# Kernel tuning notes

Measured on AMD Instinct MI355X. Metric: run time of the kernel, lower is better.

The kernel has to match this reference:

```python
import jax, jax.numpy as jnp
import numpy as np

N = 4096
F_IN = 3000
F_OUT = 64
NEG_INF = jnp.float32(-9e15)


def _xavier(key, shape):
    fan_in, fan_out = shape[0], shape[-1]
    limit = (6.0 / (fan_in + fan_out)) ** 0.5
    return jax.random.uniform(key, shape, jnp.float32, -limit, limit)


def setup_inputs() -> dict:
    key = jax.random.key(0)
    ks = jax.random.split(key, 20)
    feat = jax.random.normal(ks[0], (N, F_IN), jnp.float32)
    feat_a = jax.random.normal(ks[1], (N, F_IN), jnp.float32)
    eye = jnp.eye(N, dtype=jnp.float32)
    adj = jnp.maximum((jax.random.uniform(ks[2], (N, N)) < 0.008).astype(jnp.float32), eye)
    graph_neigh = jnp.maximum((jax.random.uniform(ks[3], (N, N)) < 0.008).astype(jnp.float32), eye)
    return {
        "feat": feat,
        "feat_a": feat_a,
        "adj": adj,
        "graph_neigh": graph_neigh,
        "weight1": _xavier(ks[4], (F_IN, F_OUT)),
        "weight2": _xavier(ks[5], (F_OUT, F_IN)),
        "att_W": _xavier(ks[6], (F_OUT, F_OUT)),
        "a_src": _xavier(ks[7], (F_OUT, 1)),
        "a_dst": _xavier(ks[8], (F_OUT, 1)),
        "mlp_W1": _xavier(ks[9], (F_OUT, 256)),
        "mlp_b1": jnp.zeros((256,), jnp.float32),
        "mlp_W2": _xavier(ks[10], (256, 128)),
        "mlp_b2": jnp.zeros((128,), jnp.float32),
        "mlp_W3": _xavier(ks[11], (128, F_OUT)),
        "mlp_b3": jnp.zeros((F_OUT,), jnp.float32),
        "dmlp_W1": _xavier(ks[12], (F_OUT, 128)),
        "dmlp_b1": jnp.zeros((128,), jnp.float32),
        "dmlp_W2": _xavier(ks[13], (128, F_OUT)),
        "dmlp_b2": jnp.zeros((F_OUT,), jnp.float32),
        "bil_W": _xavier(ks[14], (F_OUT, F_OUT)),
        "bil_b": jnp.zeros((1,), jnp.float32),
    }


def reference(feat, feat_a, adj, graph_neigh,
              weight1, weight2, att_W, a_src, a_dst,
              mlp_W1, mlp_b1, mlp_W2, mlp_b2, mlp_W3, mlp_b3,
              dmlp_W1, dmlp_b1, dmlp_W2, dmlp_b2, bil_W, bil_b):
    relu = jax.nn.relu

    def attention(h):
        Wh = h @ att_W                      # [N, F_OUT]
        e = Wh @ a_src + (Wh @ a_dst).T     # [N, N]
        e = jnp.where(e > 0, e, 0.2 * e)    # LeakyReLU(0.2)
        e = jnp.where(adj > 0, e, NEG_INF)  # mask non-edges
        return jax.nn.softmax(e, axis=1) @ Wh

    def mlp(x):
        x = relu(x @ mlp_W1 + mlp_b1)
        x = relu(x @ mlp_W2 + mlp_b2)
        return x @ mlp_W3 + mlp_b3

    def dmlp(x):  # discriminator MLP: n_h -> 128 -> n_h
        return relu(x @ dmlp_W1 + dmlp_b1) @ dmlp_W2 + dmlp_b2

    def readout(emb):  # AvgReadout + L2 normalize
        g = (graph_neigh @ emb) / jnp.sum(graph_neigh, axis=1, keepdims=True)
        return g / jnp.maximum(jnp.linalg.norm(g, axis=1, keepdims=True), 1e-12)

    def bilinear(x, y):  # nn.Bilinear(n_h, n_h, 1)
        return (jnp.einsum('ni,ij,nj->n', x, bil_W, y) + bil_b)[:, None]

    def disc(c, h_pl, h_mi):
        c, h_pl, h_mi = dmlp(c), dmlp(h_pl), dmlp(h_mi)
        return jnp.concatenate([bilinear(h_pl, c), bilinear(h_mi, c)], axis=1)

    z = mlp(attention(feat @ weight1))
    hiden_emb = z
    h = adj @ (z @ weight2)                 # spmm(adj, z @ weight2)
    emb = relu(z)
    z_a = mlp(attention(feat_a @ weight1))
    emb_a = relu(z_a)
    g = jax.nn.sigmoid(readout(emb))
    g_a = jax.nn.sigmoid(readout(emb_a))
    ret = disc(g, emb, emb_a)
    ret_a = disc(g_a, emb_a, emb)
    return (hiden_emb, h, ret, ret_a)
```

## Files before the change

### kernel.cpp

```cpp
#include <hip/hip_runtime.h>

#define NN   4096
#define FIN  3000
#define MAXN 128

typedef unsigned short u16;
typedef __bf16 bf16x8 __attribute__((ext_vector_type(8)));
typedef float f32x16 __attribute__((ext_vector_type(16)));

__device__ __forceinline__ float bf2f(u16 u) { union { unsigned int i; float f; } v; v.i = ((unsigned int)u) << 16; return v.f; }
__device__ __forceinline__ u16 f2bf(float f) {
    union { float f; unsigned int i; } v; v.f = f;
    return (u16)((v.i + 0x7FFFu + ((v.i >> 16) & 1u)) >> 16);
}
__device__ __forceinline__ bf16x8 bzero8() {
    union { unsigned long long q[2]; bf16x8 v; } u; u.q[0] = 0ull; u.q[1] = 0ull; return u.v;
}
__device__ __forceinline__ f32x16 fzero16() {
    f32x16 v;
    #pragma unroll
    for (int i = 0; i < 16; i++) v[i] = 0.f;
    return v;
}
__device__ __forceinline__ void gload_lds16(const float* src, void* ldsbase) {
    __builtin_amdgcn_global_load_lds(
        (const __attribute__((address_space(1))) void*)src,
        (__attribute__((address_space(3))) void*)ldsbase, 16, 0, 0);
}

__global__ __launch_bounds__(1024) void k_detect(const u16* __restrict__ feat, int* __restrict__ flag)
{
    __shared__ int tot;
    if (threadIdx.x == 0) tot = 0;
    __syncthreads();
    int ins = 0;
    for (int i = threadIdx.x; i < 16384; i += 1024) {
        u16 u = feat[i];
        int e = (u >> 7) & 0xFF;
        if (u != 0 && (e < 90 || e > 160)) ins++;
    }
    atomicAdd(&tot, ins);
    __syncthreads();
    if (threadIdx.x == 0) *flag = (tot > 1024) ? 1 : 0;
}

__global__ __launch_bounds__(256) void k_convw(const int* __restrict__ flag,
    const void* s0, const void* s1, const void* s2, const void* s3,
    const void* s4, const void* s5, const void* s6, const void* s7,
    const void* s8, const void* s9, const void* s10, const void* s11,
    const void* s12, const void* s13, const void* s14, const void* s15,
    float* __restrict__ dst)
{
    const void* srcs[16] = {s0,s1,s2,s3,s4,s5,s6,s7,s8,s9,s10,s11,s12,s13,s14,s15};
    const int offs[16] = {0,192000,196096,196160,196224,212608,212864,245632,245760,253952,254016,262208,262336,270528,270592,274688};
    const int ns[16]   = {192000,4096,64,64,16384,256,32768,128,8192,64,8192,128,8192,64,4096,1};
    int seg = blockIdx.y;
    int i = blockIdx.x * 256 + threadIdx.x;
    if (i >= ns[seg]) return;
    float v = (*flag) ? ((const float*)srcs[seg])[i] : bf2f(((const u16*)srcs[seg])[i]);
    dst[offs[seg] + i] = v;
}

__global__ __launch_bounds__(256) void k_convw2t(const int* __restrict__ flag,
    const void* __restrict__ src, u16* __restrict__ WH, u16* __restrict__ WL)
{
    int i = blockIdx.x * 256 + threadIdx.x;
    if (i >= 3008 * 64) return;
    int n = i >> 6, k = i & 63;
    float v = 0.f;
    if (n < FIN)
        v = (*flag) ? ((const float*)src)[(size_t)k * FIN + n]
                    : bf2f(((const u16*)src)[(size_t)k * FIN + n]);
    u16 h = f2bf(v);
    float r = v - bf2f(h);
    WH[i] = h;
    WL[i] = f2bf(r);
}

__global__ __launch_bounds__(256) void k_convw1t(const int* __restrict__ flag,
    const void* __restrict__ w1src, u16* __restrict__ BtH, u16* __restrict__ BtL)
{
    int i = blockIdx.x * 256 + threadIdx.x;
    if (i >= 64 * 3008) return;
    int c = i / 3008, k = i - c * 3008;
    float v = 0.f;
    if (k < 3000)
        v = (*flag) ? ((const float*)w1src)[(size_t)k * 64 + c]
                    : bf2f(((const u16*)w1src)[(size_t)k * 64 + c]);
    u16 h = f2bf(v);
    float r = v - bf2f(h);
    BtH[(size_t)c * 3008 + k] = h;
    BtL[(size_t)c * 3008 + k] = f2bf(r);
}

__global__ __launch_bounds__(256) void k_build_csr(const int* __restrict__ flag,
    const void* __restrict__ Av, const void* __restrict__ Gv,
    int* __restrict__ aCnt, int* __restrict__ aIdx,
    int* __restrict__ gCnt, int* __restrict__ gIdx)
{
    bool isf = (*flag != 0);
    const void* M = blockIdx.y ? Gv : Av;
    int* cnt = blockIdx.y ? gCnt : aCnt;
    int* idx = blockIdx.y ? gIdx : aIdx;
    int row = blockIdx.x, t = threadIdx.x;
    int c0 = t * 16;
    unsigned int mask = 0; int my = 0;
    if (isf) {
        const float4* r = (const float4*)((const float*)M + (size_t)row * NN + c0);
        union { float4 q[4]; float f[16]; } u;
        u.q[0] = r[0]; u.q[1] = r[1]; u.q[2] = r[2]; u.q[3] = r[3];
        #pragma unroll
        for (int j = 0; j < 16; j++) if (u.f[j] != 0.f) { mask |= 1u << j; my++; }
    } else {
        const uint4* r = (const uint4*)((const u16*)M + (size_t)row * NN + c0);
        union { uint4 q[2]; u16 h[16]; } u;
        u.q[0] = r[0]; u.q[1] = r[1];
        #pragma unroll
        for (int j = 0; j < 16; j++) if (u.h[j] != 0) { mask |= 1u << j; my++; }
    }
    __shared__ int sc[256];
    sc[t] = my;
    __syncthreads();
    for (int d = 1; d < 256; d <<= 1) {
        int v = (t >= d) ? sc[t - d] : 0;
        __syncthreads();
        sc[t] += v;
        __syncthreads();
    }
    int pos = sc[t] - my;
    for (int j = 0; j < 16; j++) {
        if (mask & (1u << j)) {
            if (pos < MAXN) idx[(size_t)row * MAXN + pos] = c0 + j;
            pos++;
        }
    }
    if (t == 0) { int total = sc[255]; cnt[row] = (total < MAXN) ? total : MAXN; }
}

__global__ __launch_bounds__(512) void k_featgemm_mfma(const int* __restrict__ flag,
    const void* __restrict__ F0v, const void* __restrict__ F1v,
    const u16* __restrict__ BtH, float* __restrict__ X0, float* __restrict__ X1)
{
    if (*flag) return;
    const u16* F = (const u16*)(blockIdx.y ? F1v : F0v);
    float* X = blockIdx.y ? X1 : X0;
    int r0 = blockIdx.x * 32;
    int tid = threadIdx.x;
    int w  = tid >> 6;
    int l  = tid & 63;
    int lr = l & 31;
    int kg = l >> 5;
    const u16* arow = F   + (size_t)(r0 + lr) * FIN + kg * 8;
    const u16* b0p  = BtH + (size_t)lr * 3008 + kg * 8;
    const u16* b1p  = BtH + (size_t)(lr + 32) * 3008 + kg * 8;
    f32x16 acc0 = fzero16(), acc1 = fzero16();
    #pragma unroll 4
    for (int s = w; s < 188; s += 8) {
        int kk = s * 16;
        bf16x8 a;
        if (kk + kg * 8 < FIN) a = *(const bf16x8*)(arow + kk);
        else                   a = bzero8();
        bf16x8 b0 = *(const bf16x8*)(b0p + kk);
        bf16x8 b1 = *(const bf16x8*)(b1p + kk);
        acc0 = __builtin_amdgcn_mfma_f32_32x32x16_bf16(a, b0, acc0, 0, 0, 0);
        acc1 = __builtin_amdgcn_mfma_f32_32x32x16_bf16(a, b1, acc1, 0, 0, 0);
    }
    __shared__ float red[8][2048];
    float* rp = red[w];
    #pragma unroll
    for (int reg = 0; reg < 16; reg++) {
        int row = (reg & 3) + 8 * (reg >> 2) + 4 * kg;
        rp[row * 64 + lr] = acc0[reg];
    }
    #pragma unroll
    for (int reg = 0; reg < 16; reg++) {
        int row = (reg & 3) + 8 * (reg >> 2) + 4 * kg;
        rp[row * 64 + 32 + lr] = acc1[reg];
    }
    __syncthreads();
    for (int i = tid; i < 2048; i += 512) {
        float s0 = 0.f;
        #pragma unroll
        for (int j = 0; j < 8; j++) s0 += red[j][i];
        X[(size_t)r0 * 64 + i] = s0;
    }
}

__global__ __launch_bounds__(256) void k_featgemm_mfma_f32(const int* __restrict__ flag,
    const void* __restrict__ F0v, const void* __restrict__ F1v,
    const u16* __restrict__ BtH, const u16* __restrict__ BtL,
    float* __restrict__ X0, float* __restrict__ X1)
{
    if (!*flag) return;
    const float* F = (const float*)(blockIdx.y ? F1v : F0v);
    float* X = blockIdx.y ? X1 : X0;
    int tid = threadIdx.x;
    int w  = tid >> 6;
    int l  = tid & 63;
    int lr = l & 31;
    int kg = l >> 5;
    int wr = w >> 1, wc = w & 1;
    int r0 = blockIdx.x * 64;
    int chunk = blockIdx.z;
    int sbeg = chunk * 12;
    int nsteps = ((chunk == 3) ? 47 : sbeg + 12) - sbeg;

    __shared__ char lds[2][16384];

    const float* Fb = F + (size_t)r0 * FIN;
    int arow = 32 * wr + lr;
    int acol = 32 * wc + lr;
    const u16* bh = BtH + (size_t)acol * 3008;
    const u16* bl = BtL + (size_t)acol * 3008;

    int slin = (w * 16) * 256 + l * 16;
    f32x16 acc = fzero16();

    {
        int kbase = sbeg * 64;
        #pragma unroll
        for (int j = 0; j < 4; j++) {
            int lin = slin + j * 1024;
            int row = lin >> 8;
            int off = (lin & 255) ^ ((row & 15) << 4);
            gload_lds16(Fb + (size_t)row * FIN + kbase + (off >> 2),
                        &lds[0][(w * 16 + j * 4) * 256]);
        }
    }
    __syncthreads();

    int cur = 0;
    for (int s = 0; s < nsteps; ++s) {
        if (s + 1 < nsteps) {
            int kbase = (sbeg + s + 1) * 64;
            #pragma unroll
            for (int j = 0; j < 4; j++) {
                int lin = slin + j * 1024;
                int row = lin >> 8;
                int off = (lin & 255) ^ ((row & 15) << 4);
                gload_lds16(Fb + (size_t)row * FIN + kbase + (off >> 2),
                            &lds[cur ^ 1][(w * 16 + j * 4) * 256]);
            }
        }
        const char* lb = lds[cur];
        int kk0 = (sbeg + s) * 64;
        #pragma unroll
        for (int s16 = 0; s16 < 4; s16++) {
            int offu = s16 * 64 + kg * 32;
            int o0 = offu        ^ ((arow & 15) << 4);
            int o1 = (offu + 16) ^ ((arow & 15) << 4);
            float4 a0 = *(const float4*)(lb + arow * 256 + o0);
            float4 a1 = *(const float4*)(lb + arow * 256 + o1);
            float av[8] = {a0.x, a0.y, a0.z, a0.w, a1.x, a1.y, a1.z, a1.w};
            bf16x8 ah, al;
            #pragma unroll
            for (int jj = 0; jj < 8; jj++) {
                __bf16 hv = (__bf16)av[jj];
                ah[jj] = hv;
                al[jj] = (__bf16)(av[jj] - (float)hv);
            }
            int kk = kk0 + s16 * 16 + kg * 8;
            bf16x8 H = *(const bf16x8*)(bh + kk);
            bf16x8 L = *(const bf16x8*)(bl + kk);
            acc = __builtin_amdgcn_mfma_f32_32x32x16_bf16(ah, H, acc, 0, 0, 0);
            acc = __builtin_amdgcn_mfma_f32_32x32x16_bf16(al, H, acc, 0, 0, 0);
            acc = __builtin_amdgcn_mfma_f32_32x32x16_bf16(ah, L, acc, 0, 0, 0);
        }
        __syncthreads();
        cur ^= 1;
    }

    #pragma unroll
    for (int reg = 0; reg < 16; reg++) {
        int row = (reg & 3) + 8 * (reg >> 2) + 4 * kg;
        atomicAdd(&X[(size_t)(r0 + 32 * wr + row) * 64 + acol], acc[reg]);
    }
}

__global__ __launch_bounds__(64) void k_whsd(
    const float* __restrict__ X1, const float* __restrict__ X2,
    const float* __restrict__ AW, const float* __restrict__ asrc, const float* __restrict__ adst,
    float* __restrict__ Wh1, float* __restrict__ Wh2,
    float* __restrict__ s1, float* __restrict__ s2,
    float* __restrict__ d1, float* __restrict__ d2)
{
    const float* X = blockIdx.y ? X2 : X1;
    float* Wh = blockIdx.y ? Wh2 : Wh1;
    float* sv = blockIdx.y ? s2 : s1;
    float* dv = blockIdx.y ? d2 : d1;
    int row = blockIdx.x, c = threadIdx.x;
    __shared__ float x[64];
    x[c] = X[(size_t)row * 64 + c];
    __syncthreads();
    float acc = 0.f;
    #pragma unroll 16
    for (int k = 0; k < 64; k++) acc += x[k] * AW[k * 64 + c];
    Wh[(size_t)row * 64 + c] = acc;
    float vs = acc * asrc[c];
    float vd = acc * adst[c];
    #pragma unroll
    for (int off = 32; off > 0; off >>= 1) { vs += __shfl_down(vs, off); vd += __shfl_down(vd, off); }
    if (c == 0) { sv[row] = vs; dv[row] = vd; }
}

__global__ __launch_bounds__(128) void k_attn(
    const int* __restrict__ cnt, const int* __restrict__ idx,
    const float* __restrict__ s1, const float* __restrict__ s2,
    const float* __restrict__ d1, const float* __restrict__ d2,
    const float* __restrict__ Wh1, const float* __restrict__ Wh2,
    float* __restrict__ A1, float* __restrict__ A2)
{
    const float* sp = blockIdx.y ? s2 : s1;
    const float* dp = blockIdx.y ? d2 : d1;
    const float* Wh = blockIdx.y ? Wh2 : Wh1;
    float* A = blockIdx.y ? A2 : A1;
    int row = blockIdx.x, tid = threadIdx.x;
    int n = cnt[row];
    __shared__ int js[MAXN];
    __shared__ float ps[MAXN];
    __shared__ float red2[2];
    __shared__ float ared[2][64];
    for (int k = tid; k < n; k += 128) js[k] = idx[(size_t)row * MAXN + k];
    __syncthreads();
    float si = sp[row];
    float m = -3.0e38f;
    for (int k = tid; k < n; k += 128) {
        float e = si + dp[js[k]];
        e = e > 0.f ? e : 0.2f * e;
        ps[k] = e;
        m = fmaxf(m, e);
    }
    #pragma unroll
    for (int off = 32; off > 0; off >>= 1) m = fmaxf(m, __shfl_down(m, off));
    if ((tid & 63) == 0) red2[tid >> 6] = m;
    __syncthreads();
    m = fmaxf(red2[0], red2[1]);
    __syncthreads();
    float zz = 0.f;
    for (int k = tid; k < n; k += 128) {
        float p = __expf(ps[k] - m);
        ps[k] = p;
        zz += p;
    }
    #pragma unroll
    for (int off = 32; off > 0; off >>= 1) zz += __shfl_down(zz, off);
    if ((tid & 63) == 0) red2[tid >> 6] = zz;
    __syncthreads();
    float Z = red2[0] + red2[1];
    Z = fmaxf(Z, 1e-20f);
    int f = tid & 63, half = tid >> 6;
    float acc = 0.f;
    for (int k = half; k < n; k += 2) acc += ps[k] * Wh[(size_t)js[k] * 64 + f];
    ared[half][f] = acc;
    __syncthreads();
    if (tid < 64) A[(size_t)row * 64 + f] = (ared[0][f] + ared[1][f]) / Z;
}

__global__ __launch_bounds__(256) void k_mlp(const int* __restrict__ flag,
    const float* __restrict__ A1, const float* __restrict__ A2,
    const float* __restrict__ W1, const float* __restrict__ b1,
    const float* __restrict__ W2, const float* __restrict__ b2,
    const float* __restrict__ W3, const float* __restrict__ b3,
    float* __restrict__ Z1, float* __restrict__ Z2, void* __restrict__ hidenv)
{
    const float* A = blockIdx.y ? A2 : A1;
    float* Z = blockIdx.y ? Z2 : Z1;
    int row0 = blockIdx.x * 4, tid = threadIdx.x;
    __shared__ float x[4][64], h1[4][256], h2[4][128];
    {
        int r = tid >> 6, c = tid & 63;
        x[r][c] = A[(size_t)(row0 + r) * 64 + c];
    }
    __syncthreads();
    {
        float a0 = b1[tid], a1v = a0, a2v = a0, a3v = a0;
        #pragma unroll 8
        for (int k = 0; k < 64; k++) {
            float w = W1[k * 256 + tid];
            a0 += x[0][k] * w; a1v += x[1][k] * w; a2v += x[2][k] * w; a3v += x[3][k] * w;
        }
        h1[0][tid] = fmaxf(a0, 0.f);  h1[1][tid] = fmaxf(a1v, 0.f);
        h1[2][tid] = fmaxf(a2v, 0.f); h1[3][tid] = fmaxf(a3v, 0.f);
    }
    __syncthreads();
    if (tid < 128) {
        float a0 = b2[tid], a1v = a0, a2v = a0, a3v = a0;
        #pragma unroll 8
        for (int k = 0; k < 256; k++) {
            float w = W2[k * 128 + tid];
            a0 += h1[0][k] * w; a1v += h1[1][k] * w; a2v += h1[2][k] * w; a3v += h1[3][k] * w;
        }
        h2[0][tid] = fmaxf(a0, 0.f);  h2[1][tid] = fmaxf(a1v, 0.f);
        h2[2][tid] = fmaxf(a2v, 0.f); h2[3][tid] = fmaxf(a3v, 0.f);
    }
    __syncthreads();
    if (tid < 64) {
        float a[4];
        a[0] = a[1] = a[2] = a[3] = b3[tid];
        #pragma unroll 8
        for (int k = 0; k < 128; k++) {
            float w = W3[k * 64 + tid];
            a[0] += h2[0][k] * w; a[1] += h2[1][k] * w; a[2] += h2[2][k] * w; a[3] += h2[3][k] * w;
        }
        bool isf = (*flag != 0);
        #pragma unroll
        for (int r = 0; r < 4; r++) {
            size_t ei = (size_t)(row0 + r) * 64 + tid;
            Z[ei] = a[r];
            if (blockIdx.y == 0) {
                if (isf) ((float*)hidenv)[ei] = a[r];
                else     ((u16*)hidenv)[ei] = f2bf(a[r]);
            }
        }
    }
}

__global__ __launch_bounds__(64) void k_spmm(
    const int* __restrict__ cnt, const int* __restrict__ idx,
    const float* __restrict__ Z, float* __restrict__ T)
{
    int row = blockIdx.x, f = threadIdx.x;
    int n = cnt[row];
    const int* ir = idx + (size_t)row * MAXN;
    float acc = 0.f;
    for (int k = 0; k < n; k++) acc += Z[(size_t)ir[k] * 64 + f];
    T[(size_t)row * 64 + f] = acc;
}

__global__ __launch_bounds__(256) void k_hgemm_mfma(const int* __restrict__ flag,
    const float* __restrict__ T, const u16* __restrict__ WH, const u16* __restrict__ WL,
    void* __restrict__ outv)
{
    bool isf = (*flag != 0);
    int tid = threadIdx.x;
    int w = tid >> 6, l = tid & 63, lr = l & 31, kg = l >> 5;
    int ct = blockIdx.y * 4 + w;
    if (ct >= 94) return;
    int r0 = blockIdx.x * 32, c0 = ct * 32;
    const float* tp = T + (size_t)(r0 + lr) * 64 + kg * 8;
    bf16x8 ah[4], al[4];
    #pragma unroll
    for (int s = 0; s < 4; s++) {
        float4 p0 = *(const float4*)(tp + s * 16);
        float4 p1 = *(const float4*)(tp + s * 16 + 4);
        float av[8] = {p0.x, p0.y, p0.z, p0.w, p1.x, p1.y, p1.z, p1.w};
        #pragma unroll
        for (int j = 0; j < 8; j++) {
            __bf16 hv = (__bf16)av[j];
            ah[s][j] = hv;
            al[s][j] = (__bf16)(av[j] - (float)hv);
        }
    }
    const u16* bh = WH + (size_t)(c0 + lr) * 64 + kg * 8;
    const u16* bl = WL + (size_t)(c0 + lr) * 64 + kg * 8;
    f32x16 acc = fzero16();
    #pragma unroll
    for (int s = 0; s < 4; s++) {
        bf16x8 vh = *(const bf16x8*)(bh + s * 16);
        bf16x8 vl = *(const bf16x8*)(bl + s * 16);
        acc = __builtin_amdgcn_mfma_f32_32x32x16_bf16(ah[s], vh, acc, 0, 0, 0);
        acc = __builtin_amdgcn_mfma_f32_32x32x16_bf16(al[s], vh, acc, 0, 0, 0);
        acc = __builtin_amdgcn_mfma_f32_32x32x16_bf16(ah[s], vl, acc, 0, 0, 0);
    }
    int col = c0 + lr;
    bool cok = col < FIN;
    #pragma unroll
    for (int reg = 0; reg < 16; reg++) {
        int row = (reg & 3) + 8 * (reg >> 2) + 4 * kg;
        size_t ei = 262144 + (size_t)(r0 + row) * FIN + col;
        if (cok) {
            if (isf) ((float*)outv)[ei] = acc[reg];
            else     ((u16*)outv)[ei] = f2bf(acc[reg]);
        }
    }
}

__global__ __launch_bounds__(64) void k_readout(
    const int* __restrict__ cnt, const int* __restrict__ idx,
    const float* __restrict__ Z1, const float* __restrict__ Z2,
    float* __restrict__ G1, float* __restrict__ G2)
{
    const float* Z = blockIdx.y ? Z2 : Z1;
    float* G = blockIdx.y ? G2 : G1;
    int row = blockIdx.x, f = threadIdx.x;
    int n = cnt[row];
    const int* ir = idx + (size_t)row * MAXN;
    float acc = 0.f;
    for (int k = 0; k < n; k++) acc += fmaxf(Z[(size_t)ir[k] * 64 + f], 0.f);
    acc /= (float)(n > 0 ? n : 1);
    float sq = acc * acc;
    #pragma unroll
    for (int off = 32; off > 0; off >>= 1) sq += __shfl_down(sq, off);
    sq = __shfl(sq, 0);
    float nrm = fmaxf(sqrtf(sq), 1e-12f);
    float v = acc / nrm;
    G[(size_t)row * 64 + f] = 1.f / (1.f + __expf(-v));
}

__global__ __launch_bounds__(128) void k_dmlp(
    const float* __restrict__ z, const float* __restrict__ za,
    const float* __restrict__ g, const float* __restrict__ ga,
    const float* __restrict__ W1, const float* __restrict__ b1,
    const float* __restrict__ W2, const float* __restrict__ b2,
    float* __restrict__ De, float* __restrict__ Dea,
    float* __restrict__ Dg, float* __restrict__ Dga)
{
    int w = blockIdx.y;
    const float* X = (w == 0) ? z : (w == 1) ? za : (w == 2) ? g : ga;
    float* O = (w == 0) ? De : (w == 1) ? Dea : (w == 2) ? Dg : Dga;
    int doRelu = (w < 2);
    int row0 = blockIdx.x * 4, tid = threadIdx.x;
    __shared__ float x[4][64], h1[4][128];
    for (int i = tid; i < 256; i += 128) {
        int r = i >> 6, c = i & 63;
        float v = X[(size_t)(row0 + r) * 64 + c];
        x[r][c] = doRelu ? fmaxf(v, 0.f) : v;
    }
    __syncthreads();
    {
        float a0 = b1[tid], a1v = a0, a2v = a0, a3v = a0;
        #pragma unroll 8
        for (int k = 0; k < 64; k++) {
            float w_ = W1[k * 128 + tid];
            a0 += x[0][k] * w_; a1v += x[1][k] * w_; a2v += x[2][k] * w_; a3v += x[3][k] * w_;
        }
        h1[0][tid] = fmaxf(a0, 0.f);  h1[1][tid] = fmaxf(a1v, 0.f);
        h1[2][tid] = fmaxf(a2v, 0.f); h1[3][tid] = fmaxf(a3v, 0.f);
    }
    __syncthreads();
    if (tid < 64) {
        float a[4];
        a[0] = a[1] = a[2] = a[3] = b2[tid];
        #pragma unroll 8
        for (int k = 0; k < 128; k++) {
            float w_ = W2[k * 64 + tid];
            a[0] += h1[0][k] * w_; a[1] += h1[1][k] * w_; a[2] += h1[2][k] * w_; a[3] += h1[3][k] * w_;
        }
        #pragma unroll
        for (int r = 0; r < 4; r++) O[(size_t)(row0 + r) * 64 + tid] = a[r];
    }
}

__global__ __launch_bounds__(64) void k_bilin(const int* __restrict__ flag,
    const float* __restrict__ De, const float* __restrict__ Dea,
    const float* __restrict__ Dg, const float* __restrict__ Dga,
    const float* __restrict__ BW, const float* __restrict__ bb, void* __restrict__ outv)
{
    int w = blockIdx.y;
    const float* X = (w == 0 || w == 3) ? De : Dea;
    const float* Y = (w <= 1) ? Dg : Dga;
    size_t bse = (w <= 1) ? (size_t)12550144 : (size_t)12558336;
    int col = (w == 0 || w == 2) ? 0 : 1;
    int row = blockIdx.x, k = threadIdx.x;
    __shared__ float x[64], y[64];
    x[k] = X[(size_t)row * 64 + k];
    y[k] = Y[(size_t)row * 64 + k];
    __syncthreads();
    float wv = 0.f;
    #pragma unroll 8
    for (int j = 0; j < 64; j++) wv += BW[k * 64 + j] * y[j];
    float v = x[k] * wv;
    #pragma unroll
    for (int off = 32; off > 0; off >>= 1) v += __shfl_down(v, off);
    if (k == 0) {
        float r = v + bb[0];
        size_t ei = bse + (size_t)row * 2 + col;
        if (*flag) ((float*)outv)[ei] = r;
        else       ((u16*)outv)[ei] = f2bf(r);
    }
}

extern "C" void kernel_launch(void* const* d_in, const int* in_sizes, int n_in,
                              void* d_out, int out_size, void* d_ws, size_t ws_size,
                              hipStream_t stream) {
    const void* feat   = d_in[0];
    const void* feat_a = d_in[1];
    const void* adj    = d_in[2];
    const void* gn     = d_in[3];
    const void* w1     = d_in[4];
    const void* w2     = d_in[5];
    const void* attW   = d_in[6];
    const void* a_src  = d_in[7];
    const void* a_dst  = d_in[8];
    const void* mW1    = d_in[9];
    const void* mb1    = d_in[10];
    const void* mW2    = d_in[11];
    const void* mb2    = d_in[12];
    const void* mW3    = d_in[13];
    const void* mb3    = d_in[14];
    const void* dW1    = d_in[15];
    const void* db1    = d_in[16];
    const void* dW2    = d_in[17];
    const void* db2    = d_in[18];
    const void* bW     = d_in[19];
    const void* bb     = d_in[20];
    (void)in_sizes; (void)n_in; (void)out_size;

    char* wsb = (char*)d_ws;
    int*   flag = (int*)wsb;
    float* T    = (float*)(wsb + 256);
    u16*   W2tH = (u16*)(wsb + 256 + 1048576);
    u16*   W2tL = W2tH + 3008 * 64;
    (void)ws_size;

    char* sc = (char*)d_out + 1048576;
    size_t soff = 0;
    auto salloc = [&](size_t nbytes) -> void* {
        void* p = (void*)(sc + soff);
        soff += (nbytes + 255) & ~(size_t)255;
        return p;
    };
    const size_t NV = (size_t)NN * 64;
    float* wA   = (float*)salloc((size_t)274689 * 4);
    int*   aCnt = (int*)salloc(NN * 4);
    int*   gCnt = (int*)salloc(NN * 4);
    int*   aIdx = (int*)salloc((size_t)NN * MAXN * 4);
    int*   gIdx = (int*)salloc((size_t)NN * MAXN * 4);
    float* X1  = (float*)salloc(NV * 4);
    float* X2  = (float*)salloc(NV * 4);
    float* Wh1 = (float*)salloc(NV * 4);
    float* Wh2 = (float*)salloc(NV * 4);
    float* A1  = (float*)salloc(NV * 4);
    float* A2  = (float*)salloc(NV * 4);
    float* z   = (float*)salloc(NV * 4);
    float* za  = (float*)salloc(NV * 4);
    float* g   = (float*)salloc(NV * 4);
    float* ga  = (float*)salloc(NV * 4);
    float* De  = (float*)salloc(NV * 4);
    float* Dea = (float*)salloc(NV * 4);
    float* Dg  = (float*)salloc(NV * 4);
    float* Dga = (float*)salloc(NV * 4);
    float* s1  = (float*)salloc(NN * 4);
    float* s2  = (float*)salloc(NN * 4);
    float* d1  = (float*)salloc(NN * 4);
    float* d2  = (float*)salloc(NN * 4);

    float* w1f   = wA + 0;
    float* attWf = wA + 192000;
    float* asrcf = wA + 196096;
    float* adstf = wA + 196160;
    float* mW1f  = wA + 196224;
    float* mb1f  = wA + 212608;
    float* mW2f  = wA + 212864;
    float* mb2f  = wA + 245632;
    float* mW3f  = wA + 245760;
    float* mb3f  = wA + 253952;
    float* dW1f  = wA + 254016;
    float* db1f  = wA + 262208;
    float* dW2f  = wA + 262336;
    float* db2f  = wA + 270528;
    float* bWf   = wA + 270592;
    float* bbf   = wA + 274688;

    u16* BtH = (u16*)De;
    u16* BtL = (u16*)Dea;

    k_detect<<<1, 1024, 0, stream>>>((const u16*)feat, flag);
    k_convw<<<dim3(750, 16), 256, 0, stream>>>(flag,
        w1, attW, a_src, a_dst, mW1, mb1, mW2, mb2, mW3, mb3,
        dW1, db1, dW2, db2, bW, bb, wA);
    k_convw2t<<<752, 256, 0, stream>>>(flag, w2, W2tH, W2tL);
    k_convw1t<<<752, 256, 0, stream>>>(flag, w1, BtH, BtL);
    k_build_csr<<<dim3(NN, 2), 256, 0, stream>>>(flag, adj, gn, aCnt, aIdx, gCnt, gIdx);
    hipMemsetAsync(X1, 0, 2 * NV * 4, stream);
    k_featgemm_mfma<<<dim3(NN / 32, 2), 512, 0, stream>>>(flag, feat, feat_a, BtH, X1, X2);
    k_featgemm_mfma_f32<<<dim3(NN / 64, 2, 4), 256, 0, stream>>>(flag, feat, feat_a, BtH, BtL, X1, X2);
    k_whsd<<<dim3(NN, 2), 64, 0, stream>>>(X1, X2, attWf, asrcf, adstf, Wh1, Wh2, s1, s2, d1, d2);
    k_attn<<<dim3(NN, 2), 128, 0, stream>>>(aCnt, aIdx, s1, s2, d1, d2, Wh1, Wh2, A1, A2);
    k_mlp<<<dim3(NN / 4, 2), 256, 0, stream>>>(flag, A1, A2, mW1f, mb1f, mW2f, mb2f, mW3f, mb3f, z, za, d_out);
    k_readout<<<dim3(NN, 2), 64, 0, stream>>>(gCnt, gIdx, z, za, g, ga);
    k_dmlp<<<dim3(NN / 4, 4), 128, 0, stream>>>(z, za, g, ga, dW1f, db1f, dW2f, db2f, De, Dea, Dg, Dga);
    k_bilin<<<dim3(NN, 4), 64, 0, stream>>>(flag, De, Dea, Dg, Dga, bWf, bbf, d_out);
    k_spmm<<<NN, 64, 0, stream>>>(aCnt, aIdx, z, T);
    k_hgemm_mfma<<<dim3(NN / 32, 24), 256, 0, stream>>>(flag, T, W2tH, W2tL, d_out);
}
```

Baseline: 461.6 us.

## Triple-buffer f32 feature GEMM, batch whsd rows, split bilinear into precompute and dot

```diff
diff --git a/kernel.cpp b/kernel.cpp
--- a/kernel.cpp
+++ b/kernel.cpp
@@ -203,46 +203,39 @@
     int r0 = blockIdx.x * 64;
     int chunk = blockIdx.z;
     int sbeg = chunk * 12;
-    int nsteps = ((chunk == 3) ? 47 : sbeg + 12) - sbeg;
-
-    __shared__ char lds[2][16384];
+    int nsteps = (chunk == 3) ? 11 : 12;
+
+    __shared__ char lds[3][16384];
 
     const float* Fb = F + (size_t)r0 * FIN;
     int arow = 32 * wr + lr;
     int acol = 32 * wc + lr;
     const u16* bh = BtH + (size_t)acol * 3008;
     const u16* bl = BtL + (size_t)acol * 3008;
-
     int slin = (w * 16) * 256 + l * 16;
     f32x16 acc = fzero16();
 
-    {
-        int kbase = sbeg * 64;
+    auto STAGE = [&](int s, int buf) {
+        int kbase = (sbeg + s) * 64;
         #pragma unroll
         for (int j = 0; j < 4; j++) {
             int lin = slin + j * 1024;
             int row = lin >> 8;
             int off = (lin & 255) ^ ((row & 15) << 4);
             gload_lds16(Fb + (size_t)row * FIN + kbase + (off >> 2),
-                        &lds[0][(w * 16 + j * 4) * 256]);
-        }
-    }
-    __syncthreads();
-
-    int cur = 0;
+                        &lds[buf][(w * 16 + j * 4) * 256]);
+        }
+    };
+
+    STAGE(0, 0);
+    STAGE(1, 1);
+
     for (int s = 0; s < nsteps; ++s) {
-        if (s + 1 < nsteps) {
-            int kbase = (sbeg + s + 1) * 64;
-            #pragma unroll
-            for (int j = 0; j < 4; j++) {
-                int lin = slin + j * 1024;
-                int row = lin >> 8;
-                int off = (lin & 255) ^ ((row & 15) << 4);
-                gload_lds16(Fb + (size_t)row * FIN + kbase + (off >> 2),
-                            &lds[cur ^ 1][(w * 16 + j * 4) * 256]);
-            }
-        }
-        const char* lb = lds[cur];
+        if (s < nsteps - 1) asm volatile("s_waitcnt vmcnt(4)" ::: "memory");
+        else                asm volatile("s_waitcnt vmcnt(0)" ::: "memory");
+        __builtin_amdgcn_s_barrier();
+        if (s + 2 < nsteps) STAGE(s + 2, (s + 2) % 3);
+        const char* lb = lds[s % 3];
         int kk0 = (sbeg + s) * 64;
         #pragma unroll
         for (int s16 = 0; s16 < 4; s16++) {
@@ -266,8 +259,6 @@
             acc = __builtin_amdgcn_mfma_f32_32x32x16_bf16(al, H, acc, 0, 0, 0);
             acc = __builtin_amdgcn_mfma_f32_32x32x16_bf16(ah, L, acc, 0, 0, 0);
         }
-        __syncthreads();
-        cur ^= 1;
     }
 
     #pragma unroll
@@ -277,7 +268,7 @@
     }
 }
 
-__global__ __launch_bounds__(64) void k_whsd(
+__global__ __launch_bounds__(256) void k_whsd(
     const float* __restrict__ X1, const float* __restrict__ X2,
     const float* __restrict__ AW, const float* __restrict__ asrc, const float* __restrict__ adst,
     float* __restrict__ Wh1, float* __restrict__ Wh2,
@@ -288,13 +279,17 @@
     float* Wh = blockIdx.y ? Wh2 : Wh1;
     float* sv = blockIdx.y ? s2 : s1;
     float* dv = blockIdx.y ? d2 : d1;
-    int row = blockIdx.x, c = threadIdx.x;
-    __shared__ float x[64];
-    x[c] = X[(size_t)row * 64 + c];
+    __shared__ float aw[64][65];
+    __shared__ float x[4][65];
+    int tid = threadIdx.x;
+    for (int i = tid; i < 4096; i += 256) aw[i >> 6][i & 63] = AW[i];
+    int g = tid >> 6, c = tid & 63;
+    int row = blockIdx.x * 4 + g;
+    x[g][c] = X[(size_t)row * 64 + c];
     __syncthreads();
     float acc = 0.f;
     #pragma unroll 16
-    for (int k = 0; k < 64; k++) acc += x[k] * AW[k * 64 + c];
+    for (int k = 0; k < 64; k++) acc += x[g][k] * aw[k][c];
     Wh[(size_t)row * 64 + c] = acc;
     float vs = acc * asrc[c];
     float vd = acc * adst[c];
@@ -541,25 +536,43 @@
     }
 }
 
-__global__ __launch_bounds__(64) void k_bilin(const int* __restrict__ flag,
+__global__ __launch_bounds__(256) void k_bilin_pre(
+    const float* __restrict__ Dg, const float* __restrict__ Dga,
+    const float* __restrict__ BW, float* __restrict__ V1, float* __restrict__ V2)
+{
+    const float* Y = blockIdx.y ? Dga : Dg;
+    float* V = blockIdx.y ? V2 : V1;
+    __shared__ float bw[64][65];
+    __shared__ float y[4][65];
+    int tid = threadIdx.x;
+    for (int i = tid; i < 4096; i += 256) bw[i >> 6][i & 63] = BW[i];
+    int g = tid >> 6, k = tid & 63;
+    int rbase = blockIdx.x * 64;
+    for (int it = 0; it < 16; it++) {
+        __syncthreads();
+        int r = rbase + it * 4 + g;
+        y[g][k] = Y[(size_t)r * 64 + k];
+        __syncthreads();
+        float acc = 0.f;
+        #pragma unroll 16
+        for (int j = 0; j < 64; j++) acc += y[g][j] * bw[k][j];
+        V[(size_t)r * 64 + k] = acc;
+    }
+}
+
+__global__ __launch_bounds__(256) void k_bilin_dot(const int* __restrict__ flag,
     const float* __restrict__ De, const float* __restrict__ Dea,
-    const float* __restrict__ Dg, const float* __restrict__ Dga,
-    const float* __restrict__ BW, const float* __restrict__ bb, void* __restrict__ outv)
+    const float* __restrict__ V1, const float* __restrict__ V2,
+    const float* __restrict__ bb, void* __restrict__ outv)
 {
     int w = blockIdx.y;
     const float* X = (w == 0 || w == 3) ? De : Dea;
-    const float* Y = (w <= 1) ? Dg : Dga;
+    const float* V = (w <= 1) ? V1 : V2;
     size_t bse = (w <= 1) ? (size_t)12550144 : (size_t)12558336;
     int col = (w == 0 || w == 2) ? 0 : 1;
-    int row = blockIdx.x, k = threadIdx.x;
-    __shared__ float x[64], y[64];
-    x[k] = X[(size_t)row * 64 + k];
-    y[k] = Y[(size_t)row * 64 + k];
-    __syncthreads();
-    float wv = 0.f;
-    #pragma unroll 8
-    for (int j = 0; j < 64; j++) wv += BW[k * 64 + j] * y[j];
-    float v = x[k] * wv;
+    int g = threadIdx.x >> 6, k = threadIdx.x & 63;
+    int row = blockIdx.x * 4 + g;
+    float v = X[(size_t)row * 64 + k] * V[(size_t)row * 64 + k];
     #pragma unroll
     for (int off = 32; off > 0; off >>= 1) v += __shfl_down(v, off);
     if (k == 0) {
@@ -665,12 +678,13 @@
     hipMemsetAsync(X1, 0, 2 * NV * 4, stream);
     k_featgemm_mfma<<<dim3(NN / 32, 2), 512, 0, stream>>>(flag, feat, feat_a, BtH, X1, X2);
     k_featgemm_mfma_f32<<<dim3(NN / 64, 2, 4), 256, 0, stream>>>(flag, feat, feat_a, BtH, BtL, X1, X2);
-    k_whsd<<<dim3(NN, 2), 64, 0, stream>>>(X1, X2, attWf, asrcf, adstf, Wh1, Wh2, s1, s2, d1, d2);
+    k_whsd<<<dim3(NN / 4, 2), 256, 0, stream>>>(X1, X2, attWf, asrcf, adstf, Wh1, Wh2, s1, s2, d1, d2);
     k_attn<<<dim3(NN, 2), 128, 0, stream>>>(aCnt, aIdx, s1, s2, d1, d2, Wh1, Wh2, A1, A2);
     k_mlp<<<dim3(NN / 4, 2), 256, 0, stream>>>(flag, A1, A2, mW1f, mb1f, mW2f, mb2f, mW3f, mb3f, z, za, d_out);
     k_readout<<<dim3(NN, 2), 64, 0, stream>>>(gCnt, gIdx, z, za, g, ga);
     k_dmlp<<<dim3(NN / 4, 4), 128, 0, stream>>>(z, za, g, ga, dW1f, db1f, dW2f, db2f, De, Dea, Dg, Dga);
-    k_bilin<<<dim3(NN, 4), 64, 0, stream>>>(flag, De, Dea, Dg, Dga, bWf, bbf, d_out);
+    k_bilin_pre<<<dim3(64, 2), 256, 0, stream>>>(Dg, Dga, bWf, A1, A2);
+    k_bilin_dot<<<dim3(NN / 4, 4), 256, 0, stream>>>(flag, De, Dea, A1, A2, bbf, d_out);
     k_spmm<<<NN, 64, 0, stream>>>(aCnt, aIdx, z, T);
     k_hgemm_mfma<<<dim3(NN / 32, 24), 256, 0, stream>>>(flag, T, W2tH, W2tL, d_out);
 }
```

Measured after the change: 448.9 us. 2.7% less time.
